# Optimization experiments

Hardware: AMD Instinct MI355X
Metric: run time of the kernel (lower is better)

Reference implementation:

```python
import jax, jax.numpy as jnp
import numpy as np

SCORE_THR = 0.05
IOU_THR = 0.5
MAX_PER_IMG = 100
PRE_NMS_K = 2048  # fixed candidate budget for jit-compatible NMS
NUM_CLASSES = 80
MEANS = jnp.array([0.0, 0.0, 0.0, 0.0], jnp.float32)
STDS = jnp.array([0.1, 0.1, 0.2, 0.2], jnp.float32)
WH_RATIO_CLIP = 16.0 / 1000.0


def setup_inputs() -> dict:
    key = jax.random.key(0)
    B, N, C = 4, 8192, NUM_CLASSES
    H, W = 800, 1333
    k1, k2, k3, k4, k5, k6 = jax.random.split(key, 6)
    class_outs = jax.random.normal(k1, (B * N, C + 1), jnp.float32)
    regression_outs = jax.random.normal(k2, (B * N, C * 4), jnp.float32) * 0.5
    x1 = jax.random.uniform(k3, (B, N), minval=0.0, maxval=W * 0.8)
    y1 = jax.random.uniform(k4, (B, N), minval=0.0, maxval=H * 0.8)
    w = jax.random.uniform(k5, (B, N), minval=8.0, maxval=W * 0.2)
    h = jax.random.uniform(k6, (B, N), minval=8.0, maxval=H * 0.2)
    boxes = jnp.stack([x1, y1, jnp.minimum(x1 + w, float(W)), jnp.minimum(y1 + h, float(H))], axis=-1)
    return {"class_outs": class_outs, "regression_outs": regression_outs, "boxes": boxes, "img_h": H, "img_w": W}


def delta2bbox(proposals, deltas, H, W):
    # proposals [N,4], deltas [N, C*4] -> decoded boxes [N, C, 4]
    d = deltas.reshape(deltas.shape[0], -1, 4) * STDS + MEANS
    dx, dy, dw, dh = d[..., 0], d[..., 1], d[..., 2], d[..., 3]
    max_ratio = jnp.abs(jnp.log(jnp.float32(WH_RATIO_CLIP)))
    dw = jnp.clip(dw, -max_ratio, max_ratio)
    dh = jnp.clip(dh, -max_ratio, max_ratio)
    px = (proposals[:, 0] + proposals[:, 2]) * 0.5
    py = (proposals[:, 1] + proposals[:, 3]) * 0.5
    pw = proposals[:, 2] - proposals[:, 0]
    ph = proposals[:, 3] - proposals[:, 1]
    gx = px[:, None] + pw[:, None] * dx
    gy = py[:, None] + ph[:, None] * dy
    gw = pw[:, None] * jnp.exp(dw)
    gh = ph[:, None] * jnp.exp(dh)
    x1 = jnp.clip(gx - gw * 0.5, 0.0, float(W))
    y1 = jnp.clip(gy - gh * 0.5, 0.0, float(H))
    x2 = jnp.clip(gx + gw * 0.5, 0.0, float(W))
    y2 = jnp.clip(gy + gh * 0.5, 0.0, float(H))
    return jnp.stack([x1, y1, x2, y2], axis=-1)


def pairwise_iou(b):
    # b [K,4] -> [K,K]
    area = jnp.maximum(b[:, 2] - b[:, 0], 0.0) * jnp.maximum(b[:, 3] - b[:, 1], 0.0)
    lt = jnp.maximum(b[:, None, :2], b[None, :, :2])
    rb = jnp.minimum(b[:, None, 2:], b[None, :, 2:])
    wh = jnp.clip(rb - lt, 0.0)
    inter = wh[..., 0] * wh[..., 1]
    union = area[:, None] + area[None, :] - inter
    return inter / jnp.maximum(union, 1e-6)


def per_image(cls_out, reg_out, props, H, W):
    C = NUM_CLASSES
    scores = jax.nn.softmax(cls_out, axis=-1)[:, :C]        # drop background column
    bboxes = delta2bbox(props[:, :4], reg_out, H, W)        # [N, C, 4]
    flat_s = scores.reshape(-1)                             # [N*C]
    flat_s = jnp.where(flat_s > SCORE_THR, flat_s, -1.0)
    top_s, top_i = jax.lax.top_k(flat_s, PRE_NMS_K)
    cand = bboxes.reshape(-1, 4)[top_i]                     # [K,4]
    labels = top_i % C
    valid = top_s > 0.0
    # class-aware NMS via coordinate offsets per class
    offset = labels.astype(cand.dtype)[:, None] * (float(max(H, W)) + 1.0)
    iou = pairwise_iou(cand + offset)                       # [K,K]
    idx = jnp.arange(PRE_NMS_K)

    def body(i, keep):
        sup = (iou[i] > IOU_THR) & (idx > i) & keep[i]
        return keep & ~sup

    keep = jax.lax.fori_loop(0, PRE_NMS_K, body, valid)
    fs = jnp.where(keep, top_s, -1.0)
    out_s, order = jax.lax.top_k(fs, MAX_PER_IMG)
    ok = out_s > 0.0
    det_boxes = jnp.where(ok[:, None], cand[order], 0.0)
    det_scores = jnp.where(ok, out_s, 0.0)
    det_labels = jnp.where(ok, labels[order], -1)
    det_inds = jnp.where(ok, top_i[order], -1)
    return det_boxes, det_scores, det_labels, det_inds


def reference(class_outs, regression_outs, boxes, img_h, img_w):
    B, N = boxes.shape[:2]
    cls = class_outs.reshape(B, N, -1)
    reg = regression_outs.reshape(B, N, -1)
    f = jax.vmap(lambda c, r, p: per_image(c, r, p, img_h, img_w))
    det_boxes, det_scores, det_labels, det_inds = f(cls, reg, boxes)
    return det_boxes, det_scores, det_labels, det_inds
```

## Files before the change

kernel.cpp:

```cpp
#include <hip/hip_runtime.h>
#include <cstdint>
#include <cstddef>

#pragma clang fp contract(off)

typedef unsigned long long u64;
typedef unsigned int u32;

#define B_IMG 4
#define N_ROI 8192
#define NCLS 80
#define NCOL 81
#define K_NMS 2048
#define MAXOUT 100
#define THR_SCORE 0.05f
#define THR_IOU 0.5f

#define NBIN 4096
#define BIN_OFF 62771u
#define RPI 2048
#define BLKCAP 128
#define STGN 4096

__device__ __forceinline__ void softmax_row(const float* __restrict__ row, int lane,
                                            float& s0, float& s1) {
  float v0 = row[lane];
  float v1 = (lane < NCOL - 64) ? row[64 + lane] : -1e38f;
  float m = fmaxf(v0, v1);
  for (int o = 32; o; o >>= 1) m = fmaxf(m, __shfl_xor(m, o));
  float e0 = expf(v0 - m);
  float e1 = (lane < NCOL - 64) ? expf(v1 - m) : 0.0f;
  float s = e0 + e1;
  for (int o = 32; o; o >>= 1) s += __shfl_xor(s, o);
  s0 = e0 / s;
  s1 = e1 / s;
}

__global__ __launch_bounds__(256) void k_score(const float* __restrict__ cls,
                                               u32* __restrict__ blkcnt,
                                               u64* __restrict__ glist) {
#pragma clang fp contract(off)
  __shared__ u32 wcnt[4];
  int t = threadIdx.x, wv = t >> 6, lane = t & 63;
  int wid = blockIdx.x * 4 + wv;
  int n = wid & (N_ROI - 1);

  float s0, s1;
  softmax_row(cls + (size_t)wid * NCOL, lane, s0, s1);
  bool c0 = s0 > THR_SCORE;
  bool c1 = (lane < 16) && (s1 > THR_SCORE);
  u64 b0 = __ballot(c0), b1 = __ballot(c1);
  int cnt = __popcll(b0) + __popcll(b1);
  if (lane == 0) wcnt[wv] = (u32)cnt;
  __syncthreads();
  u32 wbase = 0;
  for (int i = 0; i < wv; ++i) wbase += wcnt[i];
  if (t == 0) blkcnt[blockIdx.x] = wcnt[0] + wcnt[1] + wcnt[2] + wcnt[3];

  u64 lm = (1ull << lane) - 1ull;
  u64* reg = glist + (size_t)blockIdx.x * BLKCAP;
  if (c0) {
    u32 pos = wbase + (u32)__popcll(b0 & lm);
    if (pos < BLKCAP) {
      u32 flat = (u32)(n * NCLS + lane);
      reg[pos] = ((u64)__float_as_uint(s0) << 32) | (u32)(~flat);
    }
  }
  if (c1) {
    u32 pos = wbase + (u32)__popcll(b0) + (u32)__popcll(b1 & lm);
    if (pos < BLKCAP) {
      u32 flat = (u32)(n * NCLS + 64 + lane);
      reg[pos] = ((u64)__float_as_uint(s1) << 32) | (u32)(~flat);
    }
  }
}

__global__ __launch_bounds__(1024) void k_histcut(const u32* __restrict__ blkcnt,
                                                  const u64* __restrict__ glist,
                                                  u32* __restrict__ cutg,
                                                  u32* __restrict__ binbase,
                                                  u32* __restrict__ bincnt,
                                                  u32* __restrict__ keptT) {
  __shared__ u32 lh[NBIN];
  __shared__ u32 wsum[16];
  __shared__ int best;
  __shared__ u32 cutsh;
  int b = blockIdx.x, t = threadIdx.x;
  int lane = t & 63, wv = t >> 6;

  for (int i = t; i < NBIN; i += 1024) lh[i] = 0;
  __syncthreads();

  for (int r = t; r < RPI; r += 1024) {
    u32 cnt = blkcnt[b * RPI + r];
    if (cnt > BLKCAP) cnt = BLKCAP;
    const u64* reg = glist + ((size_t)(b * RPI + r)) * BLKCAP;
    for (u32 k = 0; k < cnt; ++k) {
      u64 key = reg[k];
      atomicAdd(&lh[(u32)(key >> 46) - BIN_OFF], 1u);
    }
  }
  if (t == 0) best = 0;
  __syncthreads();

  u32 v0 = lh[t * 4 + 0], v1 = lh[t * 4 + 1], v2 = lh[t * 4 + 2], v3 = lh[t * 4 + 3];
  u32 my = v0 + v1 + v2 + v3;
  u32 inc = my;
  for (int o = 1; o < 64; o <<= 1) {
    u32 x = __shfl_up(inc, o);
    if (lane >= o) inc += x;
  }
  if (lane == 63) wsum[wv] = inc;

  u32* bc = bincnt + (size_t)b * NBIN + t * 4;
  bc[0] = 0; bc[1] = 0; bc[2] = 0; bc[3] = 0;
  __syncthreads();

  u32 wpre = 0;
  for (int i = 0; i < wv; ++i) wpre += wsum[i];
  u32 total = 0;
  for (int i = 0; i < 16; ++i) total += wsum[i];
  u32 excl = wpre + (inc - my);

  u32* bb = binbase + (size_t)b * NBIN + t * 4;
  u32 pi = excl;
  pi += v0; bb[0] = total - pi;
  pi += v1; bb[1] = total - pi;
  pi += v2; bb[2] = total - pi;
  pi += v3; bb[3] = total - pi;

  if (total >= K_NMS) {
    u32 lim = total - K_NMS;
    u32 p = excl;
    int cand = -1;
    if (p <= lim) cand = t * 4 + 0; p += v0;
    if (p <= lim) cand = t * 4 + 1; p += v1;
    if (p <= lim) cand = t * 4 + 2; p += v2;
    if (p <= lim) cand = t * 4 + 3; p += v3;
    if (cand >= 0) atomicMax(&best, cand);
  }
  __syncthreads();
  if (t == 0) {
    u32 c = (total >= K_NMS) ? (u32)best : 0u;
    cutsh = c;
    cutg[b] = c;
  }
  __syncthreads();
  u32 c = cutsh;
  if (t == (int)(c >> 2)) {
    u32 pe = excl;
    int r = (int)(c & 3);
    if (r > 0) pe += v0;
    if (r > 1) pe += v1;
    if (r > 2) pe += v2;
    keptT[b] = total - pe;
  }
}

__global__ __launch_bounds__(256) void k_scatter(const u32* __restrict__ blkcnt,
                                                 const u64* __restrict__ glist,
                                                 const u32* __restrict__ cutg,
                                                 const u32* __restrict__ binbase,
                                                 u32* __restrict__ bincnt,
                                                 u64* __restrict__ staging) {
  __shared__ u32 lcnt[32];
  int blk = blockIdx.x;
  int b = blk >> 6;
  int r0 = (blk & 63) * 32;
  int t = threadIdx.x;
  if (t < 32) {
    u32 cc = blkcnt[b * RPI + r0 + t];
    lcnt[t] = (cc > BLKCAP) ? BLKCAP : cc;
  }
  __syncthreads();
  u32 cut = cutg[b];
  for (int idx = t; idx < 32 * BLKCAP; idx += 256) {
    int r = idx >> 7;
    int k = idx & (BLKCAP - 1);
    if ((u32)k < lcnt[r]) {
      u64 key = glist[((size_t)(b * RPI + r0 + r)) * BLKCAP + k];
      u32 bin = (u32)(key >> 46) - BIN_OFF;
      if (bin >= cut) {
        u32 slot = binbase[(size_t)b * NBIN + bin] +
                   atomicAdd(&bincnt[(size_t)b * NBIN + bin], 1u);
        if (slot < STGN) staging[(size_t)b * STGN + slot] = key;
      }
    }
  }
}

__global__ __launch_bounds__(256) void k_rankdecode(const u32* __restrict__ keptT,
                                                    const u32* __restrict__ binbase,
                                                    const u32* __restrict__ bincnt,
                                                    const u64* __restrict__ staging,
                                                    const float* __restrict__ props,
                                                    const float* __restrict__ regs,
                                                    const int* __restrict__ pH,
                                                    const int* __restrict__ pW,
                                                    float4* __restrict__ raw4,
                                                    float4* __restrict__ off4,
                                                    float* __restrict__ area,
                                                    float* __restrict__ scoref,
                                                    int* __restrict__ labeli,
                                                    int* __restrict__ flati) {
#pragma clang fp contract(off)
  int p0 = blockIdx.x * 256 + threadIdx.x;
  int b = p0 >> 12;
  int i = p0 & (STGN - 1);
  u32 T = keptT[b];
  if (T > STGN) T = STGN;

  if ((u32)i >= T) {
    if ((u32)i < K_NMS) {
      size_t g = (size_t)b * K_NMS + i;
      raw4[g] = make_float4(0.f, 0.f, 0.f, 0.f);
      off4[g] = make_float4(0.f, 0.f, 0.f, 0.f);
      area[g] = 0.f; scoref[g] = -1.0f; labeli[g] = 0; flati[g] = 0;
    }
    return;
  }

  u64 key = staging[(size_t)b * STGN + i];
  u32 bin = (u32)(key >> 46) - BIN_OFF;
  u32 base = binbase[(size_t)b * NBIN + bin];
  u32 cnt = bincnt[(size_t)b * NBIN + bin];
  u32 end = base + cnt;
  if (end > STGN) end = STGN;
  u32 rank = 0;
  for (u32 j = base; j < end; ++j)
    rank += (staging[(size_t)b * STGN + j] > key) ? 1u : 0u;
  u32 gslot = base + rank;
  if (gslot >= K_NMS) return;
  size_t g = (size_t)b * K_NMS + gslot;

  float Hf = (float)pH[0];
  float Wf = (float)pW[0];
  float offc = fmaxf(Hf, Wf) + 1.0f;

  u32 flat = ~(u32)(key & 0xFFFFFFFFull);
  float sc = __uint_as_float((u32)(key >> 32));
  int n = (int)(flat / NCLS);
  int c = (int)(flat - (u32)n * NCLS);

  float4 p = ((const float4*)props)[b * N_ROI + n];
  const float4 dl = *(const float4*)(regs + ((size_t)(b * N_ROI + n)) * (NCLS * 4) + c * 4);

  float mr = fabsf(logf(16.0f / 1000.0f));
  float dx = dl.x * 0.1f;
  float dy = dl.y * 0.1f;
  float dw = fminf(fmaxf(dl.z * 0.2f, -mr), mr);
  float dh = fminf(fmaxf(dl.w * 0.2f, -mr), mr);

  float px = (p.x + p.z) * 0.5f;
  float py = (p.y + p.w) * 0.5f;
  float pw = p.z - p.x;
  float ph = p.w - p.y;

  float tx = pw * dx; float gx = px + tx;
  float ty = ph * dy; float gy = py + ty;
  float gw = pw * expf(dw);
  float gh = ph * expf(dh);
  float hx = gw * 0.5f, hy = gh * 0.5f;

  float x1 = fminf(fmaxf(gx - hx, 0.0f), Wf);
  float y1 = fminf(fmaxf(gy - hy, 0.0f), Hf);
  float x2 = fminf(fmaxf(gx + hx, 0.0f), Wf);
  float y2 = fminf(fmaxf(gy + hy, 0.0f), Hf);

  raw4[g] = make_float4(x1, y1, x2, y2);

  float off = (float)c * offc;
  float ox1 = x1 + off, oy1 = y1 + off, ox2 = x2 + off, oy2 = y2 + off;
  off4[g] = make_float4(ox1, oy1, ox2, oy2);
  area[g] = fmaxf(ox2 - ox1, 0.0f) * fmaxf(oy2 - oy1, 0.0f);
  scoref[g] = sc;
  labeli[g] = c;
  flati[g] = (int)flat;
}

__global__ __launch_bounds__(256) void k_mask(const float4* __restrict__ off4,
                                              const float* __restrict__ area,
                                              u64* __restrict__ masks) {
#pragma clang fp contract(off)
  int wave = threadIdx.x >> 6, lane = threadIdx.x & 63;
  int R = blockIdx.x * 4 + wave;
  int b = R >> 11, i = R & (K_NMS - 1);
  const float4* bb = off4 + (size_t)b * K_NMS;
  const float* aa = area + (size_t)b * K_NMS;
  float4 bi = bb[i];
  float ai = aa[i];
  u64 my = 0;
  for (int w = i >> 6; w < 32; ++w) {
    int j = (w << 6) + lane;
    float4 bj = bb[j];
    float lx = fmaxf(bi.x, bj.x);
    float ly = fmaxf(bi.y, bj.y);
    float rx = fminf(bi.z, bj.z);
    float ry = fminf(bi.w, bj.w);
    float ww = fmaxf(rx - lx, 0.0f);
    float hh = fmaxf(ry - ly, 0.0f);
    float inter = ww * hh;
    float uni = (ai + aa[j]) - inter;
    float iou = inter / fmaxf(uni, 1e-6f);
    bool sup = (j > i) && (iou > THR_IOU);
    u64 word = __ballot(sup);
    if (lane == w) my = word;
  }
  if (lane < 32) masks[((size_t)R << 5) + lane] = my;
}

__global__ __launch_bounds__(64, 1) void k_scanout(const u64* __restrict__ masks,
                                                   const u32* __restrict__ keptT,
                                                   const float* __restrict__ scoref,
                                                   const float4* __restrict__ raw4,
                                                   const int* __restrict__ labeli,
                                                   const int* __restrict__ flati,
                                                   float* __restrict__ out) {
  int b = blockIdx.x;
  int lane = threadIdx.x;

  u32 Tc = keptT[b];
  if (Tc > K_NMS) Tc = K_NMS;
  u64 kw = 0;
  if (lane < 32) {
    int rem = (int)Tc - (lane << 6);
    kw = (rem >= 64) ? ~0ull : ((rem > 0) ? ((1ull << rem) - 1ull) : 0ull);
  }

  const u64* mrow = masks + ((size_t)b << 16);
  int myw = lane & 31;
  int half = lane >> 5;

  u64 dnext = mrow[((size_t)lane << 5) + 0];

  for (int c = 0; c < 32; ++c) {
    u64 dcur = dnext;
    if (c < 31) dnext = mrow[((size_t)((c + 1) * 64 + lane) << 5) + (c + 1)];

    const u64* rb = mrow + (((size_t)(c * 64 + half * 32)) << 5) + myw;
    u64 r0 = rb[0u << 5],  r1 = rb[1u << 5],  r2 = rb[2u << 5],  r3 = rb[3u << 5];
    u64 r4 = rb[4u << 5],  r5 = rb[5u << 5],  r6 = rb[6u << 5],  r7 = rb[7u << 5];
    u64 r8 = rb[8u << 5],  r9 = rb[9u << 5],  r10 = rb[10u << 5], r11 = rb[11u << 5];
    u64 r12 = rb[12u << 5], r13 = rb[13u << 5], r14 = rb[14u << 5], r15 = rb[15u << 5];
    u64 r16 = rb[16u << 5], r17 = rb[17u << 5], r18 = rb[18u << 5], r19 = rb[19u << 5];
    u64 r20 = rb[20u << 5], r21 = rb[21u << 5], r22 = rb[22u << 5], r23 = rb[23u << 5];
    u64 r24 = rb[24u << 5], r25 = rb[25u << 5], r26 = rb[26u << 5], r27 = rb[27u << 5];
    u64 r28 = rb[28u << 5], r29 = rb[29u << 5], r30 = rb[30u << 5], r31 = rb[31u << 5];
    asm volatile("" : "+v"(r0), "+v"(r1), "+v"(r2), "+v"(r3));
    asm volatile("" : "+v"(r4), "+v"(r5), "+v"(r6), "+v"(r7));
    asm volatile("" : "+v"(r8), "+v"(r9), "+v"(r10), "+v"(r11));
    asm volatile("" : "+v"(r12), "+v"(r13), "+v"(r14), "+v"(r15));
    asm volatile("" : "+v"(r16), "+v"(r17), "+v"(r18), "+v"(r19));
    asm volatile("" : "+v"(r20), "+v"(r21), "+v"(r22), "+v"(r23));
    asm volatile("" : "+v"(r24), "+v"(r25), "+v"(r26), "+v"(r27));
    asm volatile("" : "+v"(r28), "+v"(r29), "+v"(r30), "+v"(r31));

    u32 dlo = (u32)dcur, dhi = (u32)(dcur >> 32);
    u64 kc = ((u64)(u32)__builtin_amdgcn_readlane((int)(u32)(kw >> 32), c) << 32) |
             (u32)__builtin_amdgcn_readlane((int)(u32)kw, c);
#pragma unroll
    for (int d = 0; d < 64; ++d) {
      u64 dg = ((u64)(u32)__builtin_amdgcn_readlane((int)dhi, d) << 32) |
               (u32)__builtin_amdgcn_readlane((int)dlo, d);
      u64 on = (u64)0 - ((kc >> d) & 1ull);
      kc &= ~(dg & on);
    }

    u32 kb = half ? (u32)(kc >> 32) : (u32)kc;
#define ONB(r) ((u64)0 - (u64)((kb >> (r)) & 1u))
    u64 a0 = (r0 & ONB(0)) | (r1 & ONB(1)) | (r2 & ONB(2)) | (r3 & ONB(3)) |
             (r4 & ONB(4)) | (r5 & ONB(5)) | (r6 & ONB(6)) | (r7 & ONB(7));
    u64 a1 = (r8 & ONB(8)) | (r9 & ONB(9)) | (r10 & ONB(10)) | (r11 & ONB(11)) |
             (r12 & ONB(12)) | (r13 & ONB(13)) | (r14 & ONB(14)) | (r15 & ONB(15));
    u64 a2 = (r16 & ONB(16)) | (r17 & ONB(17)) | (r18 & ONB(18)) | (r19 & ONB(19)) |
             (r20 & ONB(20)) | (r21 & ONB(21)) | (r22 & ONB(22)) | (r23 & ONB(23));
    u64 a3 = (r24 & ONB(24)) | (r25 & ONB(25)) | (r26 & ONB(26)) | (r27 & ONB(27)) |
             (r28 & ONB(28)) | (r29 & ONB(29)) | (r30 & ONB(30)) | (r31 & ONB(31));
#undef ONB
    u64 supp = (a0 | a1) | (a2 | a3);
    supp |= __shfl_xor(supp, 32);
    kw &= ~supp;

    int fin = (lane <= c) ? __popcll(kw) : 0;
    for (int o = 32; o; o >>= 1) fin += __shfl_xor(fin, o);
    if (fin >= MAXOUT) break;
  }

  int pc = (lane < 32) ? __popcll(kw) : 0;
  int pre = pc;
  for (int o = 1; o < 64; o <<= 1) {
    int v = __shfl_up(pre, o);
    if (lane >= o) pre += v;
  }
  int excl = pre - pc;
  int total = __shfl(pre, 63);

  float* ob = out;
  float* os = out + B_IMG * MAXOUT * 4;
  float* ol = os + B_IMG * MAXOUT;
  float* oi = ol + B_IMG * MAXOUT;

  if (lane < 32) {
    u64 w = kw;
    int r = excl;
    while (w) {
      int bit = __ffsll((long long)w) - 1;
      w &= w - 1;
      if (r < MAXOUT) {
        int j = (lane << 6) + bit;
        size_t g = (size_t)b * K_NMS + j;
        float4 bx = raw4[g];
        int o = b * MAXOUT + r;
        ob[o * 4 + 0] = bx.x; ob[o * 4 + 1] = bx.y;
        ob[o * 4 + 2] = bx.z; ob[o * 4 + 3] = bx.w;
        os[o] = scoref[g];
        ol[o] = (float)labeli[g];
        oi[o] = (float)flati[g];
      }
      ++r;
    }
  }
  for (int r = total + lane; r < MAXOUT; r += 64) {
    int o = b * MAXOUT + r;
    ob[o * 4 + 0] = 0.f; ob[o * 4 + 1] = 0.f; ob[o * 4 + 2] = 0.f; ob[o * 4 + 3] = 0.f;
    os[o] = 0.f;
    ol[o] = -1.0f;
    oi[o] = -1.0f;
  }
}

extern "C" void kernel_launch(void* const* d_in, const int* in_sizes, int n_in,
                              void* d_out, int out_size, void* d_ws, size_t ws_size,
                              hipStream_t stream) {
  const float* cls = (const float*)d_in[0];
  const float* regs = (const float*)d_in[1];
  const float* props = (const float*)d_in[2];
  const int* pH = (const int*)d_in[3];
  const int* pW = (const int*)d_in[4];

  char* ws = (char*)d_ws;
  size_t o = 0;
  u32* blkcnt = (u32*)(ws + o); o += (size_t)B_IMG * RPI * sizeof(u32);
  u32* keptT = (u32*)(ws + o); o += 256;
  u32* cutg = (u32*)(ws + o); o += 256;
  u32* binbase = (u32*)(ws + o); o += (size_t)B_IMG * NBIN * sizeof(u32);
  u32* bincnt = (u32*)(ws + o); o += (size_t)B_IMG * NBIN * sizeof(u32);
  u64* glist = (u64*)(ws + o); o += (size_t)B_IMG * RPI * BLKCAP * sizeof(u64);
  u64* staging = (u64*)(ws + o); o += (size_t)B_IMG * STGN * sizeof(u64);
  float4* raw4 = (float4*)(ws + o); o += (size_t)B_IMG * K_NMS * sizeof(float4);
  float4* off4 = (float4*)(ws + o); o += (size_t)B_IMG * K_NMS * sizeof(float4);
  float* area = (float*)(ws + o); o += (size_t)B_IMG * K_NMS * sizeof(float);
  float* scoref = (float*)(ws + o); o += (size_t)B_IMG * K_NMS * sizeof(float);
  int* labeli = (int*)(ws + o); o += (size_t)B_IMG * K_NMS * sizeof(int);
  int* flati = (int*)(ws + o); o += (size_t)B_IMG * K_NMS * sizeof(int);
  u64* masks = (u64*)(ws + o); o += (size_t)B_IMG * K_NMS * 32 * sizeof(u64);

  k_score<<<B_IMG * RPI, 256, 0, stream>>>(cls, blkcnt, glist);
  k_histcut<<<B_IMG, 1024, 0, stream>>>(blkcnt, glist, cutg, binbase, bincnt, keptT);
  k_scatter<<<256, 256, 0, stream>>>(blkcnt, glist, cutg, binbase, bincnt, staging);
  k_rankdecode<<<B_IMG * STGN / 256, 256, 0, stream>>>(keptT, binbase, bincnt, staging,
                                                       props, regs, pH, pW,
                                                       raw4, off4, area, scoref, labeli, flati);
  k_mask<<<B_IMG * K_NMS / 4, 256, 0, stream>>>(off4, area, masks);
  k_scanout<<<B_IMG, 64, 0, stream>>>(masks, keptT, scoref, raw4, labeli, flati, (float*)d_out);
}
```

Baseline: 75.78 us.

## Build score histogram with global atomics in scoring kernel, bound scatter loop

The per-image histogram of score bins is now built inside the scoring kernel with global atomics, so the cut kernel runs only the prefix scan and no longer does a serial pass over the candidate lists in just four blocks. A small zeroing kernel clears the histogram before each run. The scatter kernel now gives each row eight threads and stops its loop at the largest row count in the block, instead of walking every slot up to capacity. This adds a kernel launch and contended global atomics on hot bins. It also leaves a dead code block in place, and the histogram counts candidates beyond the per-block cap of 128 that the list itself drops.

```diff
diff --git a/kernel.cpp b/kernel.cpp
--- a/kernel.cpp
+++ b/kernel.cpp
@@ -21,6 +21,11 @@
 #define RPI 2048
 #define BLKCAP 128
 #define STGN 4096
+
+__global__ __launch_bounds__(256) void k_zero(u32* __restrict__ p, int nwords) {
+  int i = blockIdx.x * 256 + threadIdx.x;
+  if (i < nwords) p[i] = 0;
+}
 
 __device__ __forceinline__ void softmax_row(const float* __restrict__ row, int lane,
                                             float& s0, float& s1) {
@@ -38,11 +43,13 @@
 
 __global__ __launch_bounds__(256) void k_score(const float* __restrict__ cls,
                                                u32* __restrict__ blkcnt,
-                                               u64* __restrict__ glist) {
+                                               u64* __restrict__ glist,
+                                               u32* __restrict__ hist) {
 #pragma clang fp contract(off)
   __shared__ u32 wcnt[4];
   int t = threadIdx.x, wv = t >> 6, lane = t & 63;
   int wid = blockIdx.x * 4 + wv;
+  int b = wid >> 13;
   int n = wid & (N_ROI - 1);
 
   float s0, s1;
@@ -52,6 +59,10 @@
   u64 b0 = __ballot(c0), b1 = __ballot(c1);
   int cnt = __popcll(b0) + __popcll(b1);
   if (lane == 0) wcnt[wv] = (u32)cnt;
+
+  if (c0) atomicAdd(&hist[(size_t)b * NBIN + ((__float_as_uint(s0) >> 14) - BIN_OFF)], 1u);
+  if (c1) atomicAdd(&hist[(size_t)b * NBIN + ((__float_as_uint(s1) >> 14) - BIN_OFF)], 1u);
+
   __syncthreads();
   u32 wbase = 0;
   for (int i = 0; i < wv; ++i) wbase += wcnt[i];
@@ -75,35 +86,18 @@
   }
 }
 
-__global__ __launch_bounds__(1024) void k_histcut(const u32* __restrict__ blkcnt,
-                                                  const u64* __restrict__ glist,
+__global__ __launch_bounds__(1024) void k_cutbase(const u32* __restrict__ hist,
                                                   u32* __restrict__ cutg,
                                                   u32* __restrict__ binbase,
                                                   u32* __restrict__ bincnt,
                                                   u32* __restrict__ keptT) {
-  __shared__ u32 lh[NBIN];
   __shared__ u32 wsum[16];
   __shared__ int best;
   __shared__ u32 cutsh;
   int b = blockIdx.x, t = threadIdx.x;
   int lane = t & 63, wv = t >> 6;
-
-  for (int i = t; i < NBIN; i += 1024) lh[i] = 0;
-  __syncthreads();
-
-  for (int r = t; r < RPI; r += 1024) {
-    u32 cnt = blkcnt[b * RPI + r];
-    if (cnt > BLKCAP) cnt = BLKCAP;
-    const u64* reg = glist + ((size_t)(b * RPI + r)) * BLKCAP;
-    for (u32 k = 0; k < cnt; ++k) {
-      u64 key = reg[k];
-      atomicAdd(&lh[(u32)(key >> 46) - BIN_OFF], 1u);
-    }
-  }
-  if (t == 0) best = 0;
-  __syncthreads();
-
-  u32 v0 = lh[t * 4 + 0], v1 = lh[t * 4 + 1], v2 = lh[t * 4 + 2], v3 = lh[t * 4 + 3];
+  const u32* gh = hist + (size_t)b * NBIN;
+  u32 v0 = gh[t * 4 + 0], v1 = gh[t * 4 + 1], v2 = gh[t * 4 + 2], v3 = gh[t * 4 + 3];
   u32 my = v0 + v1 + v2 + v3;
   u32 inc = my;
   for (int o = 1; o < 64; o <<= 1) {
@@ -111,6 +105,7 @@
     if (lane >= o) inc += x;
   }
   if (lane == 63) wsum[wv] = inc;
+  if (t == 0) best = 0;
 
   u32* bc = bincnt + (size_t)b * NBIN + t * 4;
   bc[0] = 0; bc[1] = 0; bc[2] = 0; bc[3] = 0;
@@ -164,6 +159,7 @@
                                                  u32* __restrict__ bincnt,
                                                  u64* __restrict__ staging) {
   __shared__ u32 lcnt[32];
+  __shared__ u32 mshare;
   int blk = blockIdx.x;
   int b = blk >> 6;
   int r0 = (blk & 63) * 32;
@@ -172,13 +168,25 @@
     u32 cc = blkcnt[b * RPI + r0 + t];
     lcnt[t] = (cc > BLKCAP) ? BLKCAP : cc;
   }
-  __syncthreads();
+  if (t < 64) {
+    u32 m = (t < 32) ? lcnt[t] : 0;
+  }
+  __syncthreads();
+  if (t == 0) {
+    u32 m = 0;
+    for (int i = 0; i < 32; ++i) m = (lcnt[i] > m) ? lcnt[i] : m;
+    mshare = m;
+  }
+  __syncthreads();
+  u32 mmax = mshare;
   u32 cut = cutg[b];
-  for (int idx = t; idx < 32 * BLKCAP; idx += 256) {
-    int r = idx >> 7;
-    int k = idx & (BLKCAP - 1);
-    if ((u32)k < lcnt[r]) {
-      u64 key = glist[((size_t)(b * RPI + r0 + r)) * BLKCAP + k];
+  int r = t >> 3;
+  int k0 = t & 7;
+  const u64* regp = glist + ((size_t)(b * RPI + r0 + r)) * BLKCAP;
+  for (u32 base = 0; base < mmax; base += 8) {
+    u32 k = base + k0;
+    if (k < lcnt[r]) {
+      u64 key = regp[k];
       u32 bin = (u32)(key >> 46) - BIN_OFF;
       if (bin >= cut) {
         u32 slot = binbase[(size_t)b * NBIN + bin] +
@@ -440,6 +448,7 @@
 
   char* ws = (char*)d_ws;
   size_t o = 0;
+  u32* hist = (u32*)(ws + o); o += (size_t)B_IMG * NBIN * sizeof(u32);
   u32* blkcnt = (u32*)(ws + o); o += (size_t)B_IMG * RPI * sizeof(u32);
   u32* keptT = (u32*)(ws + o); o += 256;
   u32* cutg = (u32*)(ws + o); o += 256;
@@ -455,8 +464,10 @@
   int* flati = (int*)(ws + o); o += (size_t)B_IMG * K_NMS * sizeof(int);
   u64* masks = (u64*)(ws + o); o += (size_t)B_IMG * K_NMS * 32 * sizeof(u64);
 
-  k_score<<<B_IMG * RPI, 256, 0, stream>>>(cls, blkcnt, glist);
-  k_histcut<<<B_IMG, 1024, 0, stream>>>(blkcnt, glist, cutg, binbase, bincnt, keptT);
+  int hist_words = B_IMG * NBIN;
+  k_zero<<<(hist_words + 255) / 256, 256, 0, stream>>>(hist, hist_words);
+  k_score<<<B_IMG * RPI, 256, 0, stream>>>(cls, blkcnt, glist, hist);
+  k_cutbase<<<B_IMG, 1024, 0, stream>>>(hist, cutg, binbase, bincnt, keptT);
   k_scatter<<<256, 256, 0, stream>>>(blkcnt, glist, cutg, binbase, bincnt, staging);
   k_rankdecode<<<B_IMG * STGN / 256, 256, 0, stream>>>(keptT, binbase, bincnt, staging,
                                                        props, regs, pH, pW,
```

After: 92.61 us. 22.2% more time.
